# Optimization experiments

Hardware: AMD Instinct MI355X
Metric: run time of the kernel (lower is better)

## Reference

```python
import jax, jax.numpy as jnp
import numpy as np

B, F, N, S, D = 128, 3, 64, 96, 64  # batch, features, nodes, steps, d_model
DIN = F + 1  # delta_t channel appended inside forward


def _layer_norm(x, g, b, eps=1e-5):
    mu = jnp.mean(x, -1, keepdims=True)
    var = jnp.mean((x - mu) ** 2, -1, keepdims=True)
    return (x - mu) * jax.lax.rsqrt(var + eps) * g + b


def _encoder_layer(x, inw, inb, ow, ob, w1, b1, w2, b2, g1, be1, g2, be2):
    # x: (B, N, D). Torch post-norm TransformerEncoderLayer, nhead=1, eval mode (no dropout).
    q, k, v = jnp.split(x @ inw.T + inb, 3, axis=-1)
    scores = jnp.einsum('bnd,bmd->bnm', q, k) / jnp.sqrt(jnp.asarray(D, x.dtype))
    a = jnp.einsum('bnm,bmd->bnd', jax.nn.softmax(scores, -1), v) @ ow.T + ob
    x = _layer_norm(x + a, g1, be1)
    ff = jax.nn.relu(x @ w1.T + b1) @ w2.T + b2
    return _layer_norm(x + ff, g2, be2)


def _diff_conv(x, adj, w, b):
    x1 = jnp.einsum('bcv,wv->bcw', x, adj)
    x2 = jnp.einsum('bcv,wv->bcw', x1, adj)
    z = jnp.concatenate([x, x1, x2], axis=1)  # (B, 3C, N)
    return jnp.einsum('bcn,oc->bon', z, w) + b[None, :, None]


def _forward(x, adj, h0, tp, uw, ub, cw, cb):
    times = x[:, 2, 0, :]  # (B, S) timestamps
    dt = jnp.concatenate([jnp.zeros((B, 1), x.dtype), times[:, 1:] - times[:, :-1]], axis=1)  # (B, S)
    xs = (jnp.transpose(x, (3, 0, 1, 2)), jnp.transpose(dt)[:, :, None])  # (S,B,F,N), (S,B,1)

    def step(h, inp):
        xt, d = inp  # (B,F,N), (B,1)
        xin = jnp.concatenate([xt, jnp.broadcast_to(d[:, :, None], (B, 1, N))], axis=1)  # (B,DIN,N)
        y = jnp.transpose(h, (0, 2, 1))  # (B, N, D): nodes are the attention sequence
        for i in range(2):
            y = _encoder_layer(y, *(a[i] for a in tp))
        eps = jnp.transpose(y, (0, 2, 1))  # (B, D, N)
        hd = jnp.sqrt(1.0 - d)[:, :, None] * h - jnp.sqrt(d)[:, :, None] * eps
        xg = jnp.concatenate([xin, hd], axis=1)  # (B, DIN+D, N)
        u = jax.nn.sigmoid(_diff_conv(xg, adj, uw, ub))
        c = jnp.tanh(_diff_conv(xg, adj, cw, cb))
        hn = u * hd + (1.0 - u) * c
        return hn, hn

    _, outs = jax.lax.scan(step, h0, xs)  # (S, B, D, N)
    return jnp.transpose(outs, (1, 3, 2, 0))  # (B, N, D, S) == stack().permute(1,3,2,0)


def setup_inputs() -> dict:
    key = jax.random.key(0)
    ks = jax.random.split(key, 12)
    s = 0.05
    x = jax.random.normal(ks[0], (B, F, N, S), jnp.float32)
    inc = jax.random.uniform(ks[1], (B, S), jnp.float32, 0.001, 0.01)
    x = x.at[:, 2, 0, :].set(jnp.cumsum(inc, axis=1))  # monotone times, delta_t in (0, 0.01)
    adj = jax.random.uniform(ks[2], (N, N), jnp.float32)
    adj = adj / jnp.sum(adj, axis=1, keepdims=True)
    h0 = jax.random.normal(ks[3], (B, D, N), jnp.float32)
    lengths = jax.random.randint(ks[4], (B,), 1, S, jnp.int32)  # unused by forward
    return {
        'x': x, 'adj': adj, 'lengths': lengths, 'h0': h0,
        't_inw': jax.random.normal(ks[5], (2, 3 * D, D), jnp.float32) * s,
        't_inb': jnp.zeros((2, 3 * D), jnp.float32),
        't_ow': jax.random.normal(ks[6], (2, D, D), jnp.float32) * s,
        't_ob': jnp.zeros((2, D), jnp.float32),
        't_w1': jax.random.normal(ks[7], (2, 64, D), jnp.float32) * s,
        't_b1': jnp.zeros((2, 64), jnp.float32),
        't_w2': jax.random.normal(ks[8], (2, D, 64), jnp.float32) * s,
        't_b2': jnp.zeros((2, D), jnp.float32),
        't_g1': jnp.ones((2, D), jnp.float32), 't_be1': jnp.zeros((2, D), jnp.float32),
        't_g2': jnp.ones((2, D), jnp.float32), 't_be2': jnp.zeros((2, D), jnp.float32),
        'uw': jax.random.normal(ks[9], (D, 3 * (DIN + D)), jnp.float32) * s,
        'ub': jnp.zeros((D,), jnp.float32),
        'cw': jax.random.normal(ks[10], (D, 3 * (DIN + D)), jnp.float32) * s,
        'cb': jnp.zeros((D,), jnp.float32),
    }


def reference(x, adj, lengths, h0, t_inw, t_inb, t_ow, t_ob, t_w1, t_b1, t_w2, t_b2,
              t_g1, t_be1, t_g2, t_be2, uw, ub, cw, cb):
    tp = (t_inw, t_inb, t_ow, t_ob, t_w1, t_b1, t_w2, t_b2, t_g1, t_be1, t_g2, t_be2)
    return _forward(x, adj, h0, tp, uw, ub, cw, cb)
```

## Files before the change

### kernel.cpp

```cpp
#include <hip/hip_runtime.h>
#include <math.h>

#define TPB 512

typedef __attribute__((ext_vector_type(8))) short bf16x8;
typedef __attribute__((ext_vector_type(4))) float f32x4;
typedef unsigned short u16;

#define MFMA(a, b, c) __builtin_amdgcn_mfma_f32_16x16x32_bf16(a, b, c, 0, 0, 0)

__device__ __forceinline__ u16 f2bf(float f) {
  union { float f; unsigned u; } v; v.f = f;
  unsigned u = v.u;
  return (u16)((u + 0x7fffu + ((u >> 16) & 1u)) >> 16);
}
__device__ __forceinline__ float bf2f(u16 h) {
  union { unsigned u; float f; } v; v.u = ((unsigned)h) << 16; return v.f;
}

__device__ __forceinline__ bf16x8 fragL(const u16* B, int row0, int pitch, int kb, int lane) {
  return *(const bf16x8*)(B + (row0 + (lane & 15)) * pitch + kb + ((lane >> 4) << 3));
}
__device__ __forceinline__ bf16x8 fragG(const float* __restrict__ W, int row0, int stride,
                                        int kb, int lane) {
  const float* p = W + (size_t)(row0 + (lane & 15)) * stride + kb + ((lane >> 4) << 3);
  float4 a = *(const float4*)p, b = *(const float4*)(p + 4);
  bf16x8 r;
  r[0] = (short)f2bf(a.x); r[1] = (short)f2bf(a.y); r[2] = (short)f2bf(a.z); r[3] = (short)f2bf(a.w);
  r[4] = (short)f2bf(b.x); r[5] = (short)f2bf(b.y); r[6] = (short)f2bf(b.z); r[7] = (short)f2bf(b.w);
  return r;
}
template<int PREW>
__device__ __forceinline__ bf16x8 wfrag(const float* __restrict__ Wg,
                                        const u16* __restrict__ Wp,
                                        int m, int f, int kh, int lane) {
  if constexpr (PREW)
    return *(const bf16x8*)(Wp + (size_t)m * 4096 + f * 1024 + kh * 512 + lane * 8);
  else
    return fragG(Wg, f * 16, 64, kh * 32, lane);
}

__global__ __launch_bounds__(256)
void prep_kernel(const float* __restrict__ t_inw, const float* __restrict__ t_ow,
                 const float* __restrict__ t_w1, const float* __restrict__ t_w2,
                 const float* __restrict__ adj, u16* __restrict__ wp) {
  int m = blockIdx.x;
  if (m == 12) {
    float* adj2 = (float*)(wp + 12 * 4096);
    for (int e = threadIdx.x; e < 4096; e += 256) {
      int w = e >> 6, u = e & 63;
      float sum = 0.f;
      for (int v = 0; v < 64; ++v) sum += adj[w * 64 + v] * adj[v * 64 + u];
      adj2[e] = sum;
    }
    return;
  }
  int l = m / 6, r = m % 6;
  const float* W;
  if (r < 3)       W = t_inw + l * 12288 + r * 4096;
  else if (r == 3) W = t_ow + l * 4096;
  else if (r == 4) W = t_w1 + l * 4096;
  else             W = t_w2 + l * 4096;
  for (int t = threadIdx.x; t < 4096; t += 256) {
    int j = t & 7, ln = (t >> 3) & 63, kh = (t >> 9) & 1, f = t >> 10;
    int row = f * 16 + (ln & 15);
    int k = kh * 32 + ((ln >> 4) << 3) + j;
    wp[(size_t)m * 4096 + t] = f2bf(W[row * 64 + k]);
  }
}

template<int PREW>
__global__ __launch_bounds__(TPB, 1)
void gcrnn_kernel(const float* __restrict__ x,
                  const float* __restrict__ adj,
                  const float* __restrict__ h0,
                  const float* __restrict__ t_inw, const float* __restrict__ t_inb,
                  const float* __restrict__ t_ow,  const float* __restrict__ t_ob,
                  const float* __restrict__ t_w1,  const float* __restrict__ t_b1,
                  const float* __restrict__ t_w2,  const float* __restrict__ t_b2,
                  const float* __restrict__ t_g1,  const float* __restrict__ t_be1,
                  const float* __restrict__ t_g2,  const float* __restrict__ t_be2,
                  const float* __restrict__ uw,    const float* __restrict__ ub,
                  const float* __restrict__ cw,    const float* __restrict__ cb,
                  const u16* __restrict__ wsW,
                  float* __restrict__ wsOut,
                  float* __restrict__ out,
                  int useStage)
{
  const int b = blockIdx.x;
  const int tid = threadIdx.x;
  const int wv = tid >> 6;
  const int lane = tid & 63;
  const int lx = lane & 15;
  const int gq = (lane >> 4) << 2;
  const int rs = wv & 3;
  const int of0 = (wv >> 2) * 2;

  __shared__ __align__(16) u16 adjB[64 * 72];
  __shared__ __align__(16) u16 adj2B[64 * 72];
  __shared__ __align__(16) u16 ysB[64 * 72];
  __shared__ __align__(16) u16 pool[4 * 4608];
  __shared__ __align__(16) u16 zTB[64 * 232];
  __shared__ __align__(16) u16 uwcwB[2 * 4 * 7 * 512];

  u16* Qb  = pool;
  u16* Kb  = pool + 4608;
  u16* VTb = pool + 9216;
  u16* Pb  = pool + 13824;
  u16* xgB = pool;

  float hreg[2][4];
  {
    const int nb = rs * 16 + gq;
#pragma unroll
    for (int ff = 0; ff < 2; ++ff) {
      int o = (of0 + ff) * 16 + lx;
      float4 hv = *(const float4*)(h0 + (size_t)b * 4096 + o * 64 + nb);
#pragma unroll
      for (int j = 0; j < 4; ++j) {
        hreg[ff][j] = (&hv.x)[j];
        ysB[(nb + j) * 72 + o] = f2bf(hreg[ff][j]);
      }
    }
  }
  for (int i = tid; i < 4096; i += TPB)
    adjB[(i >> 6) * 72 + (i & 63)] = f2bf(adj[i]);
  if constexpr (PREW) {
    const float* adj2g = (const float*)(wsW + 12 * 4096);
    for (int i = tid; i < 4096; i += TPB)
      adj2B[(i >> 6) * 72 + (i & 63)] = f2bf(adj2g[i]);
  } else {
    for (int i = tid; i < 4096; i += TPB) {
      int w = i >> 6, u = i & 63;
      float sum = 0.f;
      for (int v = 0; v < 64; ++v) sum += adj[w * 64 + v] * adj[v * 64 + u];
      adj2B[w * 72 + u] = f2bf(sum);
    }
  }
  for (int i = tid; i < 2 * 4 * 7 * 512; i += TPB) {
    int t = i;
    int j = t & 7; t >>= 3;
    int ln = t & 63; t >>= 6;
    int kh = t % 7; t /= 7;
    int f = t & 3; int mat = t >> 2;
    int o = f * 16 + (ln & 15);
    int k = kh * 32 + ((ln >> 4) << 3) + j;
    const float* W = mat ? cw : uw;
    uwcwB[i] = (k < 204) ? f2bf(W[o * 204 + k]) : (u16)0;
  }
  for (int i = tid; i < 64 * 28; i += TPB)
    zTB[(i / 28) * 232 + 204 + (i % 28)] = 0;
  __syncthreads();

  const float* times = x + ((size_t)b * 3 + 2) * 64 * 96;
  float hdreg[2][4];

  for (int s = 0; s < 96; ++s) {
    float dcur = (s == 0) ? 0.f : (times[s] - times[s - 1]);
    float sq1 = sqrtf(1.f - dcur), sq2 = sqrtf(dcur);

    for (int l = 0; l < 2; ++l) {
      const int l6 = l * 6;
      const float* inw = t_inw + l * 12288;
      const float* inb = t_inb + l * 192;
      const float* ow  = t_ow  + l * 4096;
      const float* ob  = t_ob  + l * 64;
      const float* w1  = t_w1  + l * 4096;
      const float* bb1 = t_b1  + l * 64;
      const float* w2  = t_w2  + l * 4096;
      const float* bb2 = t_b2  + l * 64;
      const float* g1  = t_g1  + l * 64;
      const float* be1 = t_be1 + l * 64;
      const float* g2  = t_g2  + l * 64;
      const float* be2 = t_be2 + l * 64;

      {
        bf16x8 a0 = fragL(ysB, rs * 16, 72, 0, lane);
        bf16x8 a1 = fragL(ysB, rs * 16, 72, 32, lane);
#pragma unroll
        for (int qk = 0; qk < 2; ++qk) {
          u16* dst = qk ? Kb : Qb;
          const float* Wg = inw + qk * 4096;
#pragma unroll
          for (int fi = 0; fi < 2; ++fi) {
            int f = (wv >> 2) + fi * 2;
            f32x4 acc = {0.f, 0.f, 0.f, 0.f};
            acc = MFMA(a0, wfrag<PREW>(Wg, wsW, l6 + qk, f, 0, lane), acc);
            acc = MFMA(a1, wfrag<PREW>(Wg, wsW, l6 + qk, f, 1, lane), acc);
            int col = f * 16 + lx;
            float bv = inb[qk * 64 + col];
#pragma unroll
            for (int j = 0; j < 4; ++j)
              dst[(rs * 16 + gq + j) * 72 + col] = f2bf(acc[j] + bv);
          }
        }
      }
      __syncthreads();

      if (wv < 4) {
        bf16x8 qa0 = fragL(Qb, rs * 16, 72, 0, lane);
        bf16x8 qa1 = fragL(Qb, rs * 16, 72, 32, lane);
        f32x4 sc[4];
#pragma unroll
        for (int f = 0; f < 4; ++f) {
          f32x4 acc = {0.f, 0.f, 0.f, 0.f};
          acc = MFMA(qa0, fragL(Kb, f * 16, 72, 0, lane), acc);
          acc = MFMA(qa1, fragL(Kb, f * 16, 72, 32, lane), acc);
#pragma unroll
          for (int j = 0; j < 4; ++j) acc[j] *= 0.125f;
          sc[f] = acc;
        }
#pragma unroll
        for (int j = 0; j < 4; ++j) {
          float m1 = fmaxf(fmaxf(sc[0][j], sc[1][j]), fmaxf(sc[2][j], sc[3][j]));
          m1 = fmaxf(m1, __shfl_xor(m1, 1));
          m1 = fmaxf(m1, __shfl_xor(m1, 2));
          m1 = fmaxf(m1, __shfl_xor(m1, 4));
          m1 = fmaxf(m1, __shfl_xor(m1, 8));
          float s1 = 0.f;
#pragma unroll
          for (int f = 0; f < 4; ++f) { float e = __expf(sc[f][j] - m1); sc[f][j] = e; s1 += e; }
          s1 += __shfl_xor(s1, 1); s1 += __shfl_xor(s1, 2);
          s1 += __shfl_xor(s1, 4); s1 += __shfl_xor(s1, 8);
          float inv = 1.f / s1;
          int row = rs * 16 + gq + j;
#pragma unroll
          for (int f = 0; f < 4; ++f)
            Pb[row * 72 + f * 16 + lx] = f2bf(sc[f][j] * inv);
        }
      } else {
        bf16x8 wa0 = wfrag<PREW>(inw + 8192, wsW, l6 + 2, rs, 0, lane);
        bf16x8 wa1 = wfrag<PREW>(inw + 8192, wsW, l6 + 2, rs, 1, lane);
#pragma unroll
        for (int f = 0; f < 4; ++f) {
          f32x4 acc = {0.f, 0.f, 0.f, 0.f};
          acc = MFMA(wa0, fragL(ysB, f * 16, 72, 0, lane), acc);
          acc = MFMA(wa1, fragL(ysB, f * 16, 72, 32, lane), acc);
#pragma unroll
          for (int j = 0; j < 4; ++j) {
            int dd = rs * 16 + gq + j;
            VTb[dd * 72 + f * 16 + lx] = f2bf(acc[j] + inb[128 + dd]);
          }
        }
      }
      __syncthreads();

      {
        bf16x8 pa0 = fragL(Pb, rs * 16, 72, 0, lane);
        bf16x8 pa1 = fragL(Pb, rs * 16, 72, 32, lane);
#pragma unroll
        for (int fi = 0; fi < 2; ++fi) {
          int f = (wv >> 2) + fi * 2;
          f32x4 acc = {0.f, 0.f, 0.f, 0.f};
          acc = MFMA(pa0, fragL(VTb, f * 16, 72, 0, lane), acc);
          acc = MFMA(pa1, fragL(VTb, f * 16, 72, 32, lane), acc);
#pragma unroll
          for (int j = 0; j < 4; ++j)
            Qb[(rs * 16 + gq + j) * 72 + f * 16 + lx] = f2bf(acc[j]);
        }
      }
      __syncthreads();

      if (wv < 4) {
        bf16x8 a0 = fragL(Qb, rs * 16, 72, 0, lane);
        bf16x8 a1 = fragL(Qb, rs * 16, 72, 32, lane);
        float t4[4][4];
#pragma unroll
        for (int f = 0; f < 4; ++f) {
          f32x4 acc = {0.f, 0.f, 0.f, 0.f};
          acc = MFMA(a0, wfrag<PREW>(ow, wsW, l6 + 3, f, 0, lane), acc);
          acc = MFMA(a1, wfrag<PREW>(ow, wsW, l6 + 3, f, 1, lane), acc);
          int col = f * 16 + lx;
          float bv = ob[col];
#pragma unroll
          for (int j = 0; j < 4; ++j) {
            int row = rs * 16 + gq + j;
            t4[f][j] = acc[j] + bv + bf2f(ysB[row * 72 + col]);
          }
        }
#pragma unroll
        for (int j = 0; j < 4; ++j) {
          float s1 = t4[0][j] + t4[1][j] + t4[2][j] + t4[3][j];
          float s2 = t4[0][j] * t4[0][j] + t4[1][j] * t4[1][j]
                   + t4[2][j] * t4[2][j] + t4[3][j] * t4[3][j];
          s1 += __shfl_xor(s1, 1); s2 += __shfl_xor(s2, 1);
          s1 += __shfl_xor(s1, 2); s2 += __shfl_xor(s2, 2);
          s1 += __shfl_xor(s1, 4); s2 += __shfl_xor(s2, 4);
          s1 += __shfl_xor(s1, 8); s2 += __shfl_xor(s2, 8);
          float mu = s1 * 0.015625f;
          float rstd = rsqrtf(s2 * 0.015625f - mu * mu + 1e-5f);
          int row = rs * 16 + gq + j;
#pragma unroll
          for (int f = 0; f < 4; ++f) {
            int col = f * 16 + lx;
            ysB[row * 72 + col] = f2bf((t4[f][j] - mu) * rstd * g1[col] + be1[col]);
          }
        }
      }
      __syncthreads();

      {
        bf16x8 a0 = fragL(ysB, rs * 16, 72, 0, lane);
        bf16x8 a1 = fragL(ysB, rs * 16, 72, 32, lane);
#pragma unroll
        for (int fi = 0; fi < 2; ++fi) {
          int f = (wv >> 2) + fi * 2;
          f32x4 acc = {0.f, 0.f, 0.f, 0.f};
          acc = MFMA(a0, wfrag<PREW>(w1, wsW, l6 + 4, f, 0, lane), acc);
          acc = MFMA(a1, wfrag<PREW>(w1, wsW, l6 + 4, f, 1, lane), acc);
          int col = f * 16 + lx;
          float bv = bb1[col];
#pragma unroll
          for (int j = 0; j < 4; ++j)
            Kb[(rs * 16 + gq + j) * 72 + col] = f2bf(fmaxf(acc[j] + bv, 0.f));
        }
      }
      __syncthreads();

      if (wv < 4) {
        bf16x8 a0 = fragL(Kb, rs * 16, 72, 0, lane);
        bf16x8 a1 = fragL(Kb, rs * 16, 72, 32, lane);
        float t4[4][4];
#pragma unroll
        for (int f = 0; f < 4; ++f) {
          f32x4 acc = {0.f, 0.f, 0.f, 0.f};
          acc = MFMA(a0, wfrag<PREW>(w2, wsW, l6 + 5, f, 0, lane), acc);
          acc = MFMA(a1, wfrag<PREW>(w2, wsW, l6 + 5, f, 1, lane), acc);
          int col = f * 16 + lx;
          float bv = bb2[col];
#pragma unroll
          for (int j = 0; j < 4; ++j) {
            int row = rs * 16 + gq + j;
            t4[f][j] = acc[j] + bv + bf2f(ysB[row * 72 + col]);
          }
        }
#pragma unroll
        for (int j = 0; j < 4; ++j) {
          float s1 = t4[0][j] + t4[1][j] + t4[2][j] + t4[3][j];
          float s2 = t4[0][j] * t4[0][j] + t4[1][j] * t4[1][j]
                   + t4[2][j] * t4[2][j] + t4[3][j] * t4[3][j];
          s1 += __shfl_xor(s1, 1); s2 += __shfl_xor(s2, 1);
          s1 += __shfl_xor(s1, 2); s2 += __shfl_xor(s2, 2);
          s1 += __shfl_xor(s1, 4); s2 += __shfl_xor(s2, 4);
          s1 += __shfl_xor(s1, 8); s2 += __shfl_xor(s2, 8);
          float mu = s1 * 0.015625f;
          float rstd = rsqrtf(s2 * 0.015625f - mu * mu + 1e-5f);
          int row = rs * 16 + gq + j;
#pragma unroll
          for (int f = 0; f < 4; ++f) {
            int col = f * 16 + lx;
            ysB[row * 72 + col] = f2bf((t4[f][j] - mu) * rstd * g2[col] + be2[col]);
          }
        }
      }
      __syncthreads();
    }

    {
      for (int i = tid; i < 256; i += TPB) {
        int f = i >> 6, n = i & 63;
        float v = (f < 3) ? x[(((size_t)b * 3 + f) * 64 + n) * 96 + s] : dcur;
        xgB[f * 72 + n] = f2bf(v);
        zTB[n * 232 + f] = f2bf(v);
      }
      const int nb = rs * 16 + gq;
#pragma unroll
      for (int ff = 0; ff < 2; ++ff) {
        int o = (of0 + ff) * 16 + lx;
        short4 hd4;
#pragma unroll
        for (int j = 0; j < 4; ++j) {
          int n = nb + j;
          float eps = bf2f(ysB[n * 72 + o]);
          float hd = sq1 * hreg[ff][j] - sq2 * eps;
          hdreg[ff][j] = hd;
          u16 hb = f2bf(hd);
          ((u16*)&hd4)[j] = hb;
          zTB[n * 232 + 4 + o] = hb;
        }
        *(short4*)(xgB + (4 + o) * 72 + nb) = hd4;
      }
    }
    __syncthreads();

    for (int t = wv; t < 40; t += 8) {
      int which = (t >= 20) ? 1 : 0;
      int tt = t - which * 20;
      int rw = tt & 3, cf = tt >> 2;
      const u16* A = which ? adj2B : adjB;
      f32x4 acc = {0.f, 0.f, 0.f, 0.f};
      acc = MFMA(fragL(A, rw * 16, 72, 0, lane), fragL(xgB, cf * 16, 72, 0, lane), acc);
      acc = MFMA(fragL(A, rw * 16, 72, 32, lane), fragL(xgB, cf * 16, 72, 32, lane), acc);
      int c = cf * 16 + lx;
      if (c < 68) {
#pragma unroll
        for (int j = 0; j < 4; ++j)
          zTB[(rw * 16 + gq + j) * 232 + 68 + which * 68 + c] = f2bf(acc[j]);
      }
    }
    __syncthreads();

    {
      f32x4 aU[2] = {{0.f,0.f,0.f,0.f},{0.f,0.f,0.f,0.f}};
      f32x4 aC[2] = {{0.f,0.f,0.f,0.f},{0.f,0.f,0.f,0.f}};
#pragma unroll
      for (int kh = 0; kh < 7; ++kh) {
        bf16x8 a = fragL(zTB, rs * 16, 232, kh * 32, lane);
#pragma unroll
        for (int ff = 0; ff < 2; ++ff) {
          int f = of0 + ff;
          const u16* pu = uwcwB + (size_t)((0 * 4 + f) * 7 + kh) * 512 + lane * 8;
          const u16* pc = uwcwB + (size_t)((1 * 4 + f) * 7 + kh) * 512 + lane * 8;
          aU[ff] = MFMA(a, *(const bf16x8*)pu, aU[ff]);
          aC[ff] = MFMA(a, *(const bf16x8*)pc, aC[ff]);
        }
      }
      const int nb = rs * 16 + gq;
#pragma unroll
      for (int ff = 0; ff < 2; ++ff) {
        int o = (of0 + ff) * 16 + lx;
        float bu_ = ub[o], bc_ = cb[o];
        float4 ov;
#pragma unroll
        for (int j = 0; j < 4; ++j) {
          int n = nb + j;
          float u = 1.f / (1.f + __expf(-(aU[ff][j] + bu_)));
          float z = aC[ff][j] + bc_;
          z = fminf(fmaxf(z, -15.f), 15.f);
          float e2 = __expf(2.f * z);
          float cval = (e2 - 1.f) / (e2 + 1.f);
          float hn = u * hdreg[ff][j] + (1.f - u) * cval;
          hreg[ff][j] = hn;
          (&ov.x)[j] = hn;
          ysB[n * 72 + o] = f2bf(hn);
        }
        if (useStage) {
          *(float4*)(wsOut + ((size_t)b * 96 + s) * 4096 + o * 64 + nb) = ov;
        } else {
#pragma unroll
          for (int j = 0; j < 4; ++j)
            out[((size_t)(b * 64 + (nb + j)) * 64 + o) * 96 + s] = (&ov.x)[j];
        }
      }
    }
    __syncthreads();
  }
}

__global__ __launch_bounds__(256)
void transp_kernel(const float* __restrict__ ws, float* __restrict__ out) {
  int blk = blockIdx.x;
  int b = blk >> 6, o = blk & 63;
  __shared__ float t[96 * 68];
  for (int i = threadIdx.x; i < 96 * 64; i += 256) {
    int ss = i >> 6, n = i & 63;
    t[ss * 68 + n] = ws[((size_t)b * 96 + ss) * 4096 + o * 64 + n];
  }
  __syncthreads();
  for (int i = threadIdx.x; i < 64 * 96; i += 256) {
    int n = i / 96, ss = i - n * 96;
    out[((size_t)(b * 64 + n) * 64 + o) * 96 + ss] = t[ss * 68 + n];
  }
}

extern "C" void kernel_launch(void* const* d_in, const int* in_sizes, int n_in,
                              void* d_out, int out_size, void* d_ws, size_t ws_size,
                              hipStream_t stream)
{
  (void)in_sizes; (void)n_in; (void)out_size;
  const float* x     = (const float*)d_in[0];
  const float* adj   = (const float*)d_in[1];
  const float* h0    = (const float*)d_in[3];
  const float* t_inw = (const float*)d_in[4];
  const float* t_inb = (const float*)d_in[5];
  const float* t_ow  = (const float*)d_in[6];
  const float* t_ob  = (const float*)d_in[7];
  const float* t_w1  = (const float*)d_in[8];
  const float* t_b1  = (const float*)d_in[9];
  const float* t_w2  = (const float*)d_in[10];
  const float* t_b2  = (const float*)d_in[11];
  const float* t_g1  = (const float*)d_in[12];
  const float* t_be1 = (const float*)d_in[13];
  const float* t_g2  = (const float*)d_in[14];
  const float* t_be2 = (const float*)d_in[15];
  const float* uw    = (const float*)d_in[16];
  const float* ub    = (const float*)d_in[17];
  const float* cw    = (const float*)d_in[18];
  const float* cb    = (const float*)d_in[19];
  float* out = (float*)d_out;

  const size_t stageBytes = (size_t)128 * 96 * 4096 * 4;
  const size_t wRegion = 12 * 4096 * 2 + 4096 * 4;
  int prew = 0, useStage = 0;
  size_t stageOff = 0;
  if (ws_size >= wRegion + stageBytes)      { prew = 1; useStage = 1; stageOff = wRegion; }
  else if (ws_size >= stageBytes)           { useStage = 1; }
  else if (ws_size >= wRegion)              { prew = 1; }

  u16* wsW = (u16*)d_ws;
  float* wsOut = (float*)((char*)d_ws + stageOff);

  if (prew)
    hipLaunchKernelGGL(prep_kernel, dim3(13), dim3(256), 0, stream,
                       t_inw, t_ow, t_w1, t_w2, adj, wsW);

  if (prew)
    hipLaunchKernelGGL(gcrnn_kernel<1>, dim3(128), dim3(TPB), 0, stream,
                       x, adj, h0, t_inw, t_inb, t_ow, t_ob, t_w1, t_b1,
                       t_w2, t_b2, t_g1, t_be1, t_g2, t_be2, uw, ub, cw, cb,
                       wsW, wsOut, out, useStage);
  else
    hipLaunchKernelGGL(gcrnn_kernel<0>, dim3(128), dim3(TPB), 0, stream,
                       x, adj, h0, t_inw, t_inb, t_ow, t_ob, t_w1, t_b1,
                       t_w2, t_b2, t_g1, t_be1, t_g2, t_be2, uw, ub, cw, cb,
                       wsW, wsOut, out, useStage);

  if (useStage)
    hipLaunchKernelGGL(transp_kernel, dim3(128 * 64), dim3(256), 0, stream, wsOut, out);
}
```

Before: 1.557 ms.

## Prefetch weight fragments early, pretranspose inputs to bf16, batch bf16 conversions

Weight fragments for Q/K/V, W1, out-projection and W2 are now loaded into registers before the preceding MFMA stages, so global/L2 latency overlaps with compute instead of stalling each matmul. A widened prep kernel precomputes per-step delta_t and a bf16 transposed copy of the input features, turning the per-step strided gather of x into a contiguous load. The launch bound changes to allow two blocks per CU and bf16 conversions are grouped. Added register pressure from held fragments and the launch-bound change could cause spills, and the new workspace layout needs a larger workspace to enable the fast path.

```diff
diff --git a/kernel.cpp b/kernel.cpp
--- a/kernel.cpp
+++ b/kernel.cpp
@@ -16,6 +16,12 @@
 }
 __device__ __forceinline__ float bf2f(u16 h) {
   union { unsigned u; float f; } v; v.u = ((unsigned)h) << 16; return v.f;
+}
+__device__ __forceinline__ unsigned cvt2(float a0, float a1) {
+  return (unsigned)f2bf(a0) | ((unsigned)f2bf(a1) << 16);
+}
+__device__ __forceinline__ void cvt4u(float a0, float a1, float a2, float a3, u16 o[4]) {
+  o[0] = f2bf(a0); o[1] = f2bf(a1); o[2] = f2bf(a2); o[3] = f2bf(a3);
 }
 
 __device__ __forceinline__ bf16x8 fragL(const u16* B, int row0, int pitch, int kb, int lane) {
@@ -43,15 +49,33 @@
 __global__ __launch_bounds__(256)
 void prep_kernel(const float* __restrict__ t_inw, const float* __restrict__ t_ow,
                  const float* __restrict__ t_w1, const float* __restrict__ t_w2,
-                 const float* __restrict__ adj, u16* __restrict__ wp) {
+                 const float* __restrict__ adj, const float* __restrict__ x,
+                 u16* __restrict__ wp, float* __restrict__ adj2,
+                 float* __restrict__ wsDT, u16* __restrict__ wsX, int doX) {
   int m = blockIdx.x;
   if (m == 12) {
-    float* adj2 = (float*)(wp + 12 * 4096);
     for (int e = threadIdx.x; e < 4096; e += 256) {
       int w = e >> 6, u = e & 63;
       float sum = 0.f;
       for (int v = 0; v < 64; ++v) sum += adj[w * 64 + v] * adj[v * 64 + u];
       adj2[e] = sum;
+    }
+    return;
+  }
+  if (m >= 13) {
+    if (!doX) return;
+    int b = m - 13;
+    const float* times = x + ((size_t)b * 3 + 2) * 64 * 96;
+    for (int i = threadIdx.x; i < 96 * 256; i += 256) {
+      int s = i >> 8, idx = i & 255, f = idx >> 6, n = idx & 63;
+      float v;
+      if (f < 3) v = x[(((size_t)b * 3 + f) * 64 + n) * 96 + s];
+      else {
+        float dt = s ? (times[s] - times[s - 1]) : 0.f;
+        v = dt;
+        if (n == 0) wsDT[b * 96 + s] = dt;
+      }
+      wsX[((size_t)b * 96 + s) * 256 + idx] = f2bf(v);
     }
     return;
   }
@@ -70,7 +94,7 @@
 }
 
 template<int PREW>
-__global__ __launch_bounds__(TPB, 1)
+__global__ __launch_bounds__(TPB, 2)
 void gcrnn_kernel(const float* __restrict__ x,
                   const float* __restrict__ adj,
                   const float* __restrict__ h0,
@@ -83,9 +107,12 @@
                   const float* __restrict__ uw,    const float* __restrict__ ub,
                   const float* __restrict__ cw,    const float* __restrict__ cb,
                   const u16* __restrict__ wsW,
+                  const float* __restrict__ adj2g,
+                  const float* __restrict__ wsDT,
+                  const u16* __restrict__ wsX,
                   float* __restrict__ wsOut,
                   float* __restrict__ out,
-                  int useStage)
+                  int useStage, int useXT)
 {
   const int b = blockIdx.x;
   const int tid = threadIdx.x;
@@ -95,6 +122,7 @@
   const int gq = (lane >> 4) << 2;
   const int rs = wv & 3;
   const int of0 = (wv >> 2) * 2;
+  const int fA = wv >> 2;
 
   __shared__ __align__(16) u16 adjB[64 * 72];
   __shared__ __align__(16) u16 adj2B[64 * 72];
@@ -126,7 +154,6 @@
   for (int i = tid; i < 4096; i += TPB)
     adjB[(i >> 6) * 72 + (i & 63)] = f2bf(adj[i]);
   if constexpr (PREW) {
-    const float* adj2g = (const float*)(wsW + 12 * 4096);
     for (int i = tid; i < 4096; i += TPB)
       adj2B[(i >> 6) * 72 + (i & 63)] = f2bf(adj2g[i]);
   } else {
@@ -156,7 +183,8 @@
   float hdreg[2][4];
 
   for (int s = 0; s < 96; ++s) {
-    float dcur = (s == 0) ? 0.f : (times[s] - times[s - 1]);
+    float dcur = useXT ? wsDT[b * 96 + s]
+                       : ((s == 0) ? 0.f : (times[s] - times[s - 1]));
     float sq1 = sqrtf(1.f - dcur), sq2 = sqrtf(dcur);
 
     for (int l = 0; l < 2; ++l) {
@@ -174,24 +202,47 @@
       const float* g2  = t_g2  + l * 64;
       const float* be2 = t_be2 + l * 64;
 
+      bf16x8 fq[2][2], fk[2][2], fw1r[2][2], fvr[2];
+#pragma unroll
+      for (int fi = 0; fi < 2; ++fi)
+#pragma unroll
+        for (int kh = 0; kh < 2; ++kh) {
+          fq[fi][kh]   = wfrag<PREW>(inw,        wsW, l6 + 0, fA + fi * 2, kh, lane);
+          fk[fi][kh]   = wfrag<PREW>(inw + 4096, wsW, l6 + 1, fA + fi * 2, kh, lane);
+          fw1r[fi][kh] = wfrag<PREW>(w1,         wsW, l6 + 4, fA + fi * 2, kh, lane);
+        }
+      if (wv >= 4) {
+#pragma unroll
+        for (int kh = 0; kh < 2; ++kh)
+          fvr[kh] = wfrag<PREW>(inw + 8192, wsW, l6 + 2, rs, kh, lane);
+      }
+
       {
         bf16x8 a0 = fragL(ysB, rs * 16, 72, 0, lane);
         bf16x8 a1 = fragL(ysB, rs * 16, 72, 32, lane);
 #pragma unroll
-        for (int qk = 0; qk < 2; ++qk) {
-          u16* dst = qk ? Kb : Qb;
-          const float* Wg = inw + qk * 4096;
-#pragma unroll
-          for (int fi = 0; fi < 2; ++fi) {
-            int f = (wv >> 2) + fi * 2;
+        for (int fi = 0; fi < 2; ++fi) {
+          int f = fA + fi * 2;
+          int col = f * 16 + lx;
+          {
             f32x4 acc = {0.f, 0.f, 0.f, 0.f};
-            acc = MFMA(a0, wfrag<PREW>(Wg, wsW, l6 + qk, f, 0, lane), acc);
-            acc = MFMA(a1, wfrag<PREW>(Wg, wsW, l6 + qk, f, 1, lane), acc);
-            int col = f * 16 + lx;
-            float bv = inb[qk * 64 + col];
+            acc = MFMA(a0, fq[fi][0], acc);
+            acc = MFMA(a1, fq[fi][1], acc);
+            float bv = inb[col];
+            u16 o4[4]; cvt4u(acc[0] + bv, acc[1] + bv, acc[2] + bv, acc[3] + bv, o4);
 #pragma unroll
             for (int j = 0; j < 4; ++j)
-              dst[(rs * 16 + gq + j) * 72 + col] = f2bf(acc[j] + bv);
+              Qb[(rs * 16 + gq + j) * 72 + col] = o4[j];
+          }
+          {
+            f32x4 acc = {0.f, 0.f, 0.f, 0.f};
+            acc = MFMA(a0, fk[fi][0], acc);
+            acc = MFMA(a1, fk[fi][1], acc);
+            float bv = inb[64 + col];
+            u16 o4[4]; cvt4u(acc[0] + bv, acc[1] + bv, acc[2] + bv, acc[3] + bv, o4);
+#pragma unroll
+            for (int j = 0; j < 4; ++j)
+              Kb[(rs * 16 + gq + j) * 72 + col] = o4[j];
           }
         }
       }
@@ -224,39 +275,50 @@
           s1 += __shfl_xor(s1, 4); s1 += __shfl_xor(s1, 8);
           float inv = 1.f / s1;
           int row = rs * 16 + gq + j;
+          u16 o4[4];
+          cvt4u(sc[0][j] * inv, sc[1][j] * inv, sc[2][j] * inv, sc[3][j] * inv, o4);
 #pragma unroll
           for (int f = 0; f < 4; ++f)
-            Pb[row * 72 + f * 16 + lx] = f2bf(sc[f][j] * inv);
+            Pb[row * 72 + f * 16 + lx] = o4[f];
         }
       } else {
-        bf16x8 wa0 = wfrag<PREW>(inw + 8192, wsW, l6 + 2, rs, 0, lane);
-        bf16x8 wa1 = wfrag<PREW>(inw + 8192, wsW, l6 + 2, rs, 1, lane);
 #pragma unroll
         for (int f = 0; f < 4; ++f) {
           f32x4 acc = {0.f, 0.f, 0.f, 0.f};
-          acc = MFMA(wa0, fragL(ysB, f * 16, 72, 0, lane), acc);
-          acc = MFMA(wa1, fragL(ysB, f * 16, 72, 32, lane), acc);
-#pragma unroll
-          for (int j = 0; j < 4; ++j) {
-            int dd = rs * 16 + gq + j;
-            VTb[dd * 72 + f * 16 + lx] = f2bf(acc[j] + inb[128 + dd]);
-          }
+          acc = MFMA(fvr[0], fragL(ysB, f * 16, 72, 0, lane), acc);
+          acc = MFMA(fvr[1], fragL(ysB, f * 16, 72, 32, lane), acc);
+          int dd0 = rs * 16 + gq;
+          u16 o4[4];
+          cvt4u(acc[0] + inb[128 + dd0], acc[1] + inb[128 + dd0 + 1],
+                acc[2] + inb[128 + dd0 + 2], acc[3] + inb[128 + dd0 + 3], o4);
+#pragma unroll
+          for (int j = 0; j < 4; ++j)
+            VTb[(dd0 + j) * 72 + f * 16 + lx] = o4[j];
         }
       }
       __syncthreads();
 
+      bf16x8 fo[4][2];
+      if (wv < 4) {
+#pragma unroll
+        for (int f = 0; f < 4; ++f)
+#pragma unroll
+          for (int kh = 0; kh < 2; ++kh)
+            fo[f][kh] = wfrag<PREW>(ow, wsW, l6 + 3, f, kh, lane);
+      }
       {
         bf16x8 pa0 = fragL(Pb, rs * 16, 72, 0, lane);
         bf16x8 pa1 = fragL(Pb, rs * 16, 72, 32, lane);
 #pragma unroll
         for (int fi = 0; fi < 2; ++fi) {
-          int f = (wv >> 2) + fi * 2;
+          int f = fA + fi * 2;
           f32x4 acc = {0.f, 0.f, 0.f, 0.f};
           acc = MFMA(pa0, fragL(VTb, f * 16, 72, 0, lane), acc);
           acc = MFMA(pa1, fragL(VTb, f * 16, 72, 32, lane), acc);
+          u16 o4[4]; cvt4u(acc[0], acc[1], acc[2], acc[3], o4);
 #pragma unroll
           for (int j = 0; j < 4; ++j)
-            Qb[(rs * 16 + gq + j) * 72 + f * 16 + lx] = f2bf(acc[j]);
+            Qb[(rs * 16 + gq + j) * 72 + f * 16 + lx] = o4[j];
         }
       }
       __syncthreads();
@@ -268,8 +330,8 @@
 #pragma unroll
         for (int f = 0; f < 4; ++f) {
           f32x4 acc = {0.f, 0.f, 0.f, 0.f};
-          acc = MFMA(a0, wfrag<PREW>(ow, wsW, l6 + 3, f, 0, lane), acc);
-          acc = MFMA(a1, wfrag<PREW>(ow, wsW, l6 + 3, f, 1, lane), acc);
+          acc = MFMA(a0, fo[f][0], acc);
+          acc = MFMA(a1, fo[f][1], acc);
           int col = f * 16 + lx;
           float bv = ob[col];
 #pragma unroll
@@ -290,29 +352,43 @@
           float mu = s1 * 0.015625f;
           float rstd = rsqrtf(s2 * 0.015625f - mu * mu + 1e-5f);
           int row = rs * 16 + gq + j;
-#pragma unroll
-          for (int f = 0; f < 4; ++f) {
-            int col = f * 16 + lx;
-            ysB[row * 72 + col] = f2bf((t4[f][j] - mu) * rstd * g1[col] + be1[col]);
-          }
+          u16 o4[4];
+          cvt4u((t4[0][j] - mu) * rstd * g1[0 * 16 + lx] + be1[0 * 16 + lx],
+                (t4[1][j] - mu) * rstd * g1[1 * 16 + lx] + be1[1 * 16 + lx],
+                (t4[2][j] - mu) * rstd * g1[2 * 16 + lx] + be1[2 * 16 + lx],
+                (t4[3][j] - mu) * rstd * g1[3 * 16 + lx] + be1[3 * 16 + lx], o4);
+#pragma unroll
+          for (int f = 0; f < 4; ++f)
+            ysB[row * 72 + f * 16 + lx] = o4[f];
         }
       }
       __syncthreads();
 
+      bf16x8 fw2[4][2];
+      if (wv < 4) {
+#pragma unroll
+        for (int f = 0; f < 4; ++f)
+#pragma unroll
+          for (int kh = 0; kh < 2; ++kh)
+            fw2[f][kh] = wfrag<PREW>(w2, wsW, l6 + 5, f, kh, lane);
+      }
       {
         bf16x8 a0 = fragL(ysB, rs * 16, 72, 0, lane);
         bf16x8 a1 = fragL(ysB, rs * 16, 72, 32, lane);
 #pragma unroll
         for (int fi = 0; fi < 2; ++fi) {
-          int f = (wv >> 2) + fi * 2;
+          int f = fA + fi * 2;
           f32x4 acc = {0.f, 0.f, 0.f, 0.f};
-          acc = MFMA(a0, wfrag<PREW>(w1, wsW, l6 + 4, f, 0, lane), acc);
-          acc = MFMA(a1, wfrag<PREW>(w1, wsW, l6 + 4, f, 1, lane), acc);
+          acc = MFMA(a0, fw1r[fi][0], acc);
+          acc = MFMA(a1, fw1r[fi][1], acc);
           int col = f * 16 + lx;
           float bv = bb1[col];
+          u16 o4[4];
+          cvt4u(fmaxf(acc[0] + bv, 0.f), fmaxf(acc[1] + bv, 0.f),
+                fmaxf(acc[2] + bv, 0.f), fmaxf(acc[3] + bv, 0.f), o4);
 #pragma unroll
           for (int j = 0; j < 4; ++j)
-            Kb[(rs * 16 + gq + j) * 72 + col] = f2bf(fmaxf(acc[j] + bv, 0.f));
+            Kb[(rs * 16 + gq + j) * 72 + col] = o4[j];
         }
       }
       __syncthreads();
@@ -324,8 +400,8 @@
 #pragma unroll
         for (int f = 0; f < 4; ++f) {
           f32x4 acc = {0.f, 0.f, 0.f, 0.f};
-          acc = MFMA(a0, wfrag<PREW>(w2, wsW, l6 + 5, f, 0, lane), acc);
-          acc = MFMA(a1, wfrag<PREW>(w2, wsW, l6 + 5, f, 1, lane), acc);
+          acc = MFMA(a0, fw2[f][0], acc);
+          acc = MFMA(a1, fw2[f][1], acc);
           int col = f * 16 + lx;
           float bv = bb2[col];
 #pragma unroll
@@ -346,39 +422,53 @@
           float mu = s1 * 0.015625f;
           float rstd = rsqrtf(s2 * 0.015625f - mu * mu + 1e-5f);
           int row = rs * 16 + gq + j;
-#pragma unroll
-          for (int f = 0; f < 4; ++f) {
-            int col = f * 16 + lx;
-            ysB[row * 72 + col] = f2bf((t4[f][j] - mu) * rstd * g2[col] + be2[col]);
-          }
+          u16 o4[4];
+          cvt4u((t4[0][j] - mu) * rstd * g2[0 * 16 + lx] + be2[0 * 16 + lx],
+                (t4[1][j] - mu) * rstd * g2[1 * 16 + lx] + be2[1 * 16 + lx],
+                (t4[2][j] - mu) * rstd * g2[2 * 16 + lx] + be2[2 * 16 + lx],
+                (t4[3][j] - mu) * rstd * g2[3 * 16 + lx] + be2[3 * 16 + lx], o4);
+#pragma unroll
+          for (int f = 0; f < 4; ++f)
+            ysB[row * 72 + f * 16 + lx] = o4[f];
         }
       }
       __syncthreads();
     }
 
     {
-      for (int i = tid; i < 256; i += TPB) {
-        int f = i >> 6, n = i & 63;
-        float v = (f < 3) ? x[(((size_t)b * 3 + f) * 64 + n) * 96 + s] : dcur;
-        xgB[f * 72 + n] = f2bf(v);
-        zTB[n * 232 + f] = f2bf(v);
+      if (useXT) {
+        const u16* xr = wsX + ((size_t)b * 96 + s) * 256;
+        for (int i = tid; i < 256; i += TPB) {
+          u16 v = xr[i];
+          int f = i >> 6, n = i & 63;
+          xgB[f * 72 + n] = v;
+          zTB[n * 232 + f] = v;
+        }
+      } else {
+        for (int i = tid; i < 256; i += TPB) {
+          int f = i >> 6, n = i & 63;
+          float v = (f < 3) ? x[(((size_t)b * 3 + f) * 64 + n) * 96 + s] : dcur;
+          u16 v16 = f2bf(v);
+          xgB[f * 72 + n] = v16;
+          zTB[n * 232 + f] = v16;
+        }
       }
       const int nb = rs * 16 + gq;
 #pragma unroll
       for (int ff = 0; ff < 2; ++ff) {
         int o = (of0 + ff) * 16 + lx;
-        short4 hd4;
-#pragma unroll
-        for (int j = 0; j < 4; ++j) {
-          int n = nb + j;
-          float eps = bf2f(ysB[n * 72 + o]);
-          float hd = sq1 * hreg[ff][j] - sq2 * eps;
-          hdreg[ff][j] = hd;
-          u16 hb = f2bf(hd);
-          ((u16*)&hd4)[j] = hb;
-          zTB[n * 232 + 4 + o] = hb;
-        }
-        *(short4*)(xgB + (4 + o) * 72 + nb) = hd4;
+        float hd0 = sq1 * hreg[ff][0] - sq2 * bf2f(ysB[(nb + 0) * 72 + o]);
+        float hd1 = sq1 * hreg[ff][1] - sq2 * bf2f(ysB[(nb + 1) * 72 + o]);
+        float hd2 = sq1 * hreg[ff][2] - sq2 * bf2f(ysB[(nb + 2) * 72 + o]);
+        float hd3 = sq1 * hreg[ff][3] - sq2 * bf2f(ysB[(nb + 3) * 72 + o]);
+        hdreg[ff][0] = hd0; hdreg[ff][1] = hd1; hdreg[ff][2] = hd2; hdreg[ff][3] = hd3;
+        unsigned p0 = cvt2(hd0, hd1), p1 = cvt2(hd2, hd3);
+        zTB[(nb + 0) * 232 + 4 + o] = (u16)p0;
+        zTB[(nb + 1) * 232 + 4 + o] = (u16)(p0 >> 16);
+        zTB[(nb + 2) * 232 + 4 + o] = (u16)p1;
+        zTB[(nb + 3) * 232 + 4 + o] = (u16)(p1 >> 16);
+        uint2 pk; pk.x = p0; pk.y = p1;
+        *(uint2*)(xgB + (4 + o) * 72 + nb) = pk;
       }
     }
     __syncthreads();
@@ -393,9 +483,10 @@
       acc = MFMA(fragL(A, rw * 16, 72, 32, lane), fragL(xgB, cf * 16, 72, 32, lane), acc);
       int c = cf * 16 + lx;
       if (c < 68) {
+        u16 o4[4]; cvt4u(acc[0], acc[1], acc[2], acc[3], o4);
 #pragma unroll
         for (int j = 0; j < 4; ++j)
-          zTB[(rw * 16 + gq + j) * 232 + 68 + which * 68 + c] = f2bf(acc[j]);
+          zTB[(rw * 16 + gq + j) * 232 + 68 + which * 68 + c] = o4[j];
       }
     }
     __syncthreads();
@@ -423,7 +514,6 @@
         float4 ov;
 #pragma unroll
         for (int j = 0; j < 4; ++j) {
-          int n = nb + j;
           float u = 1.f / (1.f + __expf(-(aU[ff][j] + bu_)));
           float z = aC[ff][j] + bc_;
           z = fminf(fmaxf(z, -15.f), 15.f);
@@ -432,8 +522,12 @@
           float hn = u * hdreg[ff][j] + (1.f - u) * cval;
           hreg[ff][j] = hn;
           (&ov.x)[j] = hn;
-          ysB[n * 72 + o] = f2bf(hn);
-        }
+        }
+        unsigned pk0 = cvt2(ov.x, ov.y), pk1 = cvt2(ov.z, ov.w);
+        ysB[(nb + 0) * 72 + o] = (u16)pk0;
+        ysB[(nb + 1) * 72 + o] = (u16)(pk0 >> 16);
+        ysB[(nb + 2) * 72 + o] = (u16)pk1;
+        ysB[(nb + 3) * 72 + o] = (u16)(pk1 >> 16);
         if (useStage) {
           *(float4*)(wsOut + ((size_t)b * 96 + s) * 4096 + o * 64 + nb) = ov;
         } else {
@@ -489,31 +583,39 @@
   const float* cb    = (const float*)d_in[19];
   float* out = (float*)d_out;
 
+  const size_t offAdj2 = 98304;
+  const size_t offDT   = 114688;
+  const size_t offX    = 163840;
+  const size_t offStageFull = 6455296;
   const size_t stageBytes = (size_t)128 * 96 * 4096 * 4;
-  const size_t wRegion = 12 * 4096 * 2 + 4096 * 4;
-  int prew = 0, useStage = 0;
+
+  int prew = 0, useStage = 0, useXT = 0;
   size_t stageOff = 0;
-  if (ws_size >= wRegion + stageBytes)      { prew = 1; useStage = 1; stageOff = wRegion; }
+  if (ws_size >= offStageFull + stageBytes) { prew = 1; useXT = 1; useStage = 1; stageOff = offStageFull; }
+  else if (ws_size >= offX + stageBytes)    { prew = 1; useStage = 1; stageOff = offX; }
   else if (ws_size >= stageBytes)           { useStage = 1; }
-  else if (ws_size >= wRegion)              { prew = 1; }
-
-  u16* wsW = (u16*)d_ws;
+  else if (ws_size >= offX)                 { prew = 1; }
+
+  u16*   wsW   = (u16*)d_ws;
+  float* adj2g = (float*)((char*)d_ws + offAdj2);
+  float* wsDT  = (float*)((char*)d_ws + offDT);
+  u16*   wsX   = (u16*)((char*)d_ws + offX);
   float* wsOut = (float*)((char*)d_ws + stageOff);
 
   if (prew)
-    hipLaunchKernelGGL(prep_kernel, dim3(13), dim3(256), 0, stream,
-                       t_inw, t_ow, t_w1, t_w2, adj, wsW);
+    hipLaunchKernelGGL(prep_kernel, dim3(13 + (useXT ? 128 : 0)), dim3(256), 0, stream,
+                       t_inw, t_ow, t_w1, t_w2, adj, x, wsW, adj2g, wsDT, wsX, useXT);
 
   if (prew)
     hipLaunchKernelGGL(gcrnn_kernel<1>, dim3(128), dim3(TPB), 0, stream,
                        x, adj, h0, t_inw, t_inb, t_ow, t_ob, t_w1, t_b1,
                        t_w2, t_b2, t_g1, t_be1, t_g2, t_be2, uw, ub, cw, cb,
-                       wsW, wsOut, out, useStage);
+                       wsW, adj2g, wsDT, wsX, wsOut, out, useStage, useXT);
   else
     hipLaunchKernelGGL(gcrnn_kernel<0>, dim3(128), dim3(TPB), 0, stream,
                        x, adj, h0, t_inw, t_inb, t_ow, t_ob, t_w1, t_b1,
                        t_w2, t_b2, t_g1, t_be1, t_g2, t_be2, uw, ub, cw, cb,
-                       wsW, wsOut, out, useStage);
+                       wsW, adj2g, wsDT, wsX, wsOut, out, useStage, 0);
 
   if (useStage)
     hipLaunchKernelGGL(transp_kernel, dim3(128 * 64), dim3(256), 0, stream, wsOut, out);
```

Result: slower. 1.599 ms (+2.7%).
